# Kernel optimization log

Hardware: AMD Instinct MI355X
Metric: run time of the kernel (lower is better)

## Reference

```python
import jax, jax.numpy as jnp
import numpy as np

N_NODES = 50000
N_EDGES = 150000
N_GRAPHS = 1024
IN_DIM = 78
OUT_DIM = 64
HEADS = 10
HID = OUT_DIM * HEADS  # 640
NEG_SLOPE = 0.2


def _add_self_loops(edge_index, num_nodes):
    loop = jnp.arange(num_nodes, dtype=edge_index.dtype)
    src = jnp.concatenate([edge_index[0], loop])
    dst = jnp.concatenate([edge_index[1], loop])
    return src, dst


def gatv2_conv(x, edge_index, Wl, Wr, att, bias, heads, out_dim):
    # PyG GATv2Conv (share_weights=False, concat=True, add_self_loops=True),
    # inference mode so attention dropout is a no-op.
    N = x.shape[0]
    src, dst = _add_self_loops(edge_index, N)
    xl = (x @ Wl).reshape(N, heads, out_dim)  # source transform
    xr = (x @ Wr).reshape(N, heads, out_dim)  # target transform
    s = jax.nn.leaky_relu(xl[src] + xr[dst], NEG_SLOPE)      # [E,H,C]
    logits = jnp.einsum('ehc,hc->eh', s, att)                # [E,H]
    m = jax.ops.segment_max(logits, dst, num_segments=N)     # [N,H] (self-loops => no empty segs)
    ex = jnp.exp(logits - m[dst])
    den = jax.ops.segment_sum(ex, dst, num_segments=N)
    alpha = ex / den[dst]                                    # scatter-softmax over in-edges
    out = jax.ops.segment_sum(alpha[:, :, None] * xl[src], dst, num_segments=N)
    return out.reshape(N, heads * out_dim) + bias


def gcn_conv(x, edge_index, W, b):
    N = x.shape[0]
    src, dst = _add_self_loops(edge_index, N)
    deg = jax.ops.segment_sum(jnp.ones(src.shape[0], x.dtype), dst, num_segments=N)
    dinv = jax.lax.rsqrt(jnp.maximum(deg, 1.0))
    norm = dinv[src] * dinv[dst]                             # [E]
    xw = x @ W
    return jax.ops.segment_sum(norm[:, None] * xw[src], dst, num_segments=N) + b


def setup_inputs() -> dict:
    key = jax.random.key(0)
    ks = jax.random.split(key, 16)
    x = jax.random.normal(ks[0], (N_NODES, IN_DIM), dtype=jnp.float32)
    edge_index = jax.random.randint(ks[1], (2, N_EDGES), 0, N_NODES, dtype=jnp.int64)
    batch = jnp.sort(jax.random.randint(ks[2], (N_NODES,), 0, N_GRAPHS, dtype=jnp.int64))

    def glorot(k, shape, fan_in):
        return jax.random.normal(k, shape, dtype=jnp.float32) * (1.0 / np.sqrt(fan_in))

    return {
        'x': x, 'edge_index': edge_index, 'batch': batch,
        'Wl1': glorot(ks[3], (IN_DIM, HID), IN_DIM),
        'Wr1': glorot(ks[4], (IN_DIM, HID), IN_DIM),
        'a1': glorot(ks[5], (HEADS, OUT_DIM), OUT_DIM),
        'b1': jnp.zeros((HID,), jnp.float32),
        'Wl2': glorot(ks[6], (HID, HID), HID),
        'Wr2': glorot(ks[7], (HID, HID), HID),
        'a2': glorot(ks[8], (1, HID), HID),
        'b2': jnp.zeros((HID,), jnp.float32),
        'Wg': glorot(ks[9], (HID, HID), HID),
        'bg': jnp.zeros((HID,), jnp.float32),
    }


def reference(x, edge_index, batch, Wl1, Wr1, a1, b1, Wl2, Wr2, a2, b2, Wg, bg):
    # inference: feature dropout layers are identity
    h = jax.nn.elu(gatv2_conv(x, edge_index, Wl1, Wr1, a1, b1, HEADS, OUT_DIM))
    h = gatv2_conv(h, edge_index, Wl2, Wr2, a2, b2, 1, HID)
    h = gcn_conv(h, edge_index, Wg, bg)
    h = jax.nn.relu(h)
    # global max pool + global mean pool per graph
    gmax = jax.ops.segment_max(h, batch, num_segments=N_GRAPHS)
    cnt = jax.ops.segment_sum(jnp.ones((h.shape[0],), h.dtype), batch, num_segments=N_GRAPHS)
    gmean = jax.ops.segment_sum(h, batch, num_segments=N_GRAPHS) / jnp.maximum(cnt, 1.0)[:, None]
    return jnp.concatenate([gmax, gmean], axis=1)
```

## Files before the change

### kernel.cpp

```cpp
#include <hip/hip_runtime.h>
#include <hip/hip_bf16.h>
#include <cstdint>
#include <cstddef>

typedef __hip_bfloat16 bf16;

#define N_NODES  50000
#define N_EDGES  150000
#define E_TOT    (N_EDGES + N_NODES)
#define N_TILES  ((E_TOT + 15) / 16)
#define N_GRAPHS 1024
#define IN_DIM   78
#define K1P      128
#define OUT_DIM  64
#define HEADS    10
#define HID      640
#define NEG_SLOPE 0.2f
#define SCB      ((N_NODES + 255) / 256)

static __device__ __forceinline__ float b2f(bf16 v){ return __bfloat162float(v); }
static __device__ __forceinline__ bf16  f2b(float v){ return __float2bfloat16(v); }

__device__ __forceinline__ int clampi(int v, int hi){ return v < 0 ? 0 : (v >= hi ? hi - 1 : v); }

__device__ __forceinline__ float bf2f_bits(short s){
  return __uint_as_float(((unsigned)(unsigned short)s) << 16);
}
__device__ __forceinline__ short f2bf_bits(float v){
  unsigned u = __float_as_uint(v);
  return (short)((u + 0x7fffu + ((u >> 16) & 1u)) >> 16);
}
__device__ __forceinline__ short f2bf_trunc(float v){
  return (short)(__float_as_uint(v) >> 16);
}

__global__ __launch_bounds__(256) void fill_u32(unsigned* __restrict__ p, unsigned v, int n){
  int i = blockIdx.x * 256 + threadIdx.x;
  if (i < n) p[i] = v;
}

__global__ __launch_bounds__(256) void conv_x(const float* __restrict__ x, bf16* __restrict__ XB){
  int i = blockIdx.x * 256 + threadIdx.x;
  if (i >= N_NODES * K1P) return;
  int n = i / K1P, k = i - n * K1P;
  XB[i] = f2b(k < IN_DIM ? x[(size_t)n * IN_DIM + k] : 0.f);
}

__global__ __launch_bounds__(256) void conv_wT2(const float* __restrict__ W0,
                                                const float* __restrict__ W1,
                                                bf16* __restrict__ WT,
                                                int K, int N, int Kp){
  int i = blockIdx.x * 256 + threadIdx.x;
  const int per = N * Kp;
  if (i >= 2 * per) return;
  int m = i / per, r = i - m * per;
  const float* W = m == 0 ? W0 : W1;
  int n = r / Kp, k = r - n * Kp;
  WT[i] = f2b(k < K ? W[(size_t)k * N + n] : 0.f);
}

__global__ __launch_bounds__(256) void conv_wT3t(const float* __restrict__ W0,
                                                 const float* __restrict__ W1,
                                                 const float* __restrict__ W2,
                                                 bf16* __restrict__ WT){
  __shared__ float t[32][33];
  int m = blockIdx.z;
  const float* W = m == 0 ? W0 : (m == 1 ? W1 : W2);
  int n0 = blockIdx.x * 32, k0 = blockIdx.y * 32;
  int tx = threadIdx.x & 31, ty = threadIdx.x >> 5;
#pragma unroll
  for (int r = 0; r < 32; r += 8)
    t[ty + r][tx] = W[(size_t)(k0 + ty + r) * HID + n0 + tx];
  __syncthreads();
  bf16* O = WT + (size_t)m * HID * HID;
#pragma unroll
  for (int r = 0; r < 32; r += 8)
    O[(size_t)(n0 + ty + r) * HID + k0 + tx] = f2b(t[tx][ty + r]);
}

__global__ __launch_bounds__(256) void conv_attP(const float* __restrict__ a, bf16* __restrict__ P,
                                                 int heads){
  int i = blockIdx.x * 256 + threadIdx.x;
  if (i >= (HID / 32) * 512) return;
  int chunk = i >> 9;
  int lane  = (i >> 3) & 63;
  int j     = i & 7;
  int h = lane & 15;
  int k = (lane >> 4) * 8 + j;
  int c = chunk * 32 + k;
  float v = 0.f;
  if (heads == HEADS){ if (h < HEADS && (c >> 6) == h) v = a[c]; }
  else               { if (h == 0) v = a[c]; }
  P[i] = f2b(v);
}

#define BM 128
#define BN 128
#define BK 64

typedef __attribute__((ext_vector_type(8))) short bf16x8;
typedef __attribute__((ext_vector_type(4))) float f32x4;

typedef const __attribute__((address_space(1))) unsigned gu32;
typedef __attribute__((address_space(3))) unsigned lu32;

__global__ __launch_bounds__(256) void mfma_gemm(const bf16* __restrict__ A,
                                                 const bf16* __restrict__ BT,
                                                 bf16* __restrict__ C0,
                                                 bf16* __restrict__ C1,
                                                 int M, int Kp, int NB){
  int d   = blockIdx.x;
  int xcd = d & 7, j = d >> 3;
  int cb  = j % NB, ri = j / NB;
  int rb  = ri * 8 + xcd;
  const int row0 = rb * BM;
  if (row0 >= M) return;
  const int col0 = cb * BN;

  __shared__ short As[BM * BK];
  __shared__ short Bs[BN * BK];
  const int tid  = threadIdx.x;
  const int lane = tid & 63;
  const int wave = tid >> 6;
  const int wr   = (wave >> 1) * 64;
  const int wc   = (wave & 1) * 64;
  const int l15  = lane & 15;
  const int quad = lane >> 4;
  const int sw   = l15 & 7;

  const bf16* aptr[4];
  const bf16* bptr[4];
  lu32* lda[4];
  lu32* ldb[4];
#pragma unroll
  for (int t = 0; t < 4; ++t){
    int ci = (t * 4 + wave) * 64 + lane;
    int r  = ci >> 3;
    int sc = (ci & 7) ^ (r & 7);
    int gr = row0 + r; if (gr >= M) gr = M - 1;
    aptr[t] = A  + (size_t)gr * Kp + sc * 8;
    bptr[t] = BT + (size_t)(col0 + r) * Kp + sc * 8;
    lda[t]  = (lu32*)(&As[(t * 4 + wave) * 512]);
    ldb[t]  = (lu32*)(&Bs[(t * 4 + wave) * 512]);
  }

  f32x4 acc[4][4];
#pragma unroll
  for (int i = 0; i < 4; ++i)
#pragma unroll
    for (int jj = 0; jj < 4; ++jj) acc[i][jj] = (f32x4){0.f, 0.f, 0.f, 0.f};

  for (int k0 = 0; k0 < Kp; k0 += BK){
#pragma unroll
    for (int t = 0; t < 4; ++t){
      __builtin_amdgcn_global_load_lds((gu32*)(aptr[t] + k0), lda[t], 16, 0, 0);
      __builtin_amdgcn_global_load_lds((gu32*)(bptr[t] + k0), ldb[t], 16, 0, 0);
    }
    __syncthreads();

#pragma unroll
    for (int ks = 0; ks < 2; ++ks){
      const int slotA = ((ks * 4 + quad) ^ sw) * 8;
      bf16x8 af[4], bfr[4];
#pragma unroll
      for (int i = 0; i < 4; ++i)
        af[i] = *(bf16x8*)(&As[(wr + i * 16 + l15) * BK + slotA]);
#pragma unroll
      for (int jj = 0; jj < 4; ++jj)
        bfr[jj] = *(bf16x8*)(&Bs[(wc + jj * 16 + l15) * BK + slotA]);
#pragma unroll
      for (int i = 0; i < 4; ++i)
#pragma unroll
        for (int jj = 0; jj < 4; ++jj)
          acc[i][jj] = __builtin_amdgcn_mfma_f32_16x16x32_bf16(af[i], bfr[jj], acc[i][jj], 0, 0, 0);
    }
    __syncthreads();
  }

  if (row0 + BM <= M){
#pragma unroll
    for (int i = 0; i < 4; ++i){
#pragma unroll
      for (int jj = 0; jj < 4; ++jj){
        int gc = col0 + wc + jj * 16 + l15;
        bf16* Cp = (gc < HID) ? C0 : C1;
        size_t cc = (gc < HID) ? gc : gc - HID;
        size_t base = (size_t)(row0 + wr + i * 16 + quad * 4) * HID + cc;
#pragma unroll
        for (int r = 0; r < 4; ++r)
          Cp[base + (size_t)r * HID] = f2b(acc[i][jj][r]);
      }
    }
  } else {
#pragma unroll
    for (int i = 0; i < 4; ++i){
#pragma unroll
      for (int jj = 0; jj < 4; ++jj){
        int gc = col0 + wc + jj * 16 + l15;
        bf16* Cp = (gc < HID) ? C0 : C1;
        int cc   = (gc < HID) ? gc : gc - HID;
#pragma unroll
        for (int r = 0; r < 4; ++r){
          int gr = row0 + wr + i * 16 + quad * 4 + r;
          if (gr < M) Cp[(size_t)gr * HID + cc] = f2b(acc[i][jj][r]);
        }
      }
    }
  }
}

__global__ __launch_bounds__(256) void count_deg(const int* __restrict__ edst, int* __restrict__ degi){
  int e = blockIdx.x * 256 + threadIdx.x;
  if (e >= N_EDGES) return;
  atomicAdd(&degi[clampi(edst[e], N_NODES)], 1);
}

__global__ __launch_bounds__(256) void scan_blk(const int* __restrict__ degi,
                                                int* __restrict__ rowp,
                                                float* __restrict__ dinv,
                                                int* __restrict__ bsum){
  __shared__ int wsum[4];
  int b = blockIdx.x, tid = threadIdx.x;
  int i = b * 256 + tid;
  int lane = tid & 63, wv = tid >> 6;
  int v = (i < N_NODES) ? degi[i] : 0;
  int incl = v;
#pragma unroll
  for (int ofs = 1; ofs < 64; ofs <<= 1){
    int t = __shfl_up(incl, ofs);
    if (lane >= ofs) incl += t;
  }
  if (lane == 63) wsum[wv] = incl;
  __syncthreads();
  int woff = 0;
#pragma unroll
  for (int w = 0; w < 4; ++w) if (w < wv) woff += wsum[w];
  if (i < N_NODES){
    rowp[i] = woff + incl - v;
    dinv[i] = rsqrtf((float)(v + 1));
  }
  if (tid == 0) bsum[b] = wsum[0] + wsum[1] + wsum[2] + wsum[3];
}

__global__ __launch_bounds__(256) void scan_top(int* __restrict__ bsum, int* __restrict__ rowp){
  __shared__ int wsum[4];
  int tid = threadIdx.x, lane = tid & 63, wv = tid >> 6;
  int v = (tid < SCB) ? bsum[tid] : 0;
  int incl = v;
#pragma unroll
  for (int ofs = 1; ofs < 64; ofs <<= 1){
    int t = __shfl_up(incl, ofs);
    if (lane >= ofs) incl += t;
  }
  if (lane == 63) wsum[wv] = incl;
  __syncthreads();
  int woff = 0;
#pragma unroll
  for (int w = 0; w < 4; ++w) if (w < wv) woff += wsum[w];
  if (tid < SCB) bsum[tid] = woff + incl - v;
  if (tid == 255) rowp[N_NODES] = woff + incl;
}

__global__ __launch_bounds__(256) void scan_add(const int* __restrict__ bsum,
                                                int* __restrict__ rowp,
                                                int* __restrict__ curs){
  int i = blockIdx.x * 256 + threadIdx.x;
  if (i >= N_NODES) return;
  int r = rowp[i] + bsum[blockIdx.x];
  rowp[i] = r; curs[i] = r;
}

__global__ __launch_bounds__(256) void bucket_edges(const int* __restrict__ esrc,
                                                    const int* __restrict__ edst,
                                                    int* __restrict__ curs,
                                                    int* __restrict__ srcg,
                                                    int* __restrict__ dstg){
  int e = blockIdx.x * 256 + threadIdx.x;
  if (e >= N_EDGES) return;
  int d = clampi(edst[e], N_NODES);
  int pos = atomicAdd(&curs[d], 1);
  srcg[pos] = clampi(esrc[e], N_NODES);
  dstg[pos] = d;
}

__global__ __launch_bounds__(256) void logits_mfma(const bf16* __restrict__ xl,
                                                   const bf16* __restrict__ xr,
                                                   const int* __restrict__ srcg,
                                                   const int* __restrict__ dstg,
                                                   const bf16* __restrict__ attP,
                                                   float* __restrict__ LOG,
                                                   int only0){
  int wid  = (blockIdx.x * 256 + threadIdx.x) >> 6;
  int lane = threadIdx.x & 63;
  if (wid >= N_TILES) return;
  const int l15 = lane & 15, quad = lane >> 4;
  int p = wid * 16 + l15; if (p >= E_TOT) p = E_TOT - 1;
  int s, d;
  if (p < N_EDGES){ s = srcg[p]; d = dstg[p]; }
  else            { s = d = p - N_EDGES; }
  const bf16* ps = xl + (size_t)s * HID + quad * 8;
  const bf16* pd = xr + (size_t)d * HID + quad * 8;
  const bf16* pw = attP + lane * 8;

  f32x4 acc = (f32x4){0.f, 0.f, 0.f, 0.f};
  for (int k0 = 0; k0 < HID; k0 += 64){
    bf16x8 va0 = *(const bf16x8*)(ps + k0);
    bf16x8 vb0 = *(const bf16x8*)(pd + k0);
    bf16x8 va1 = *(const bf16x8*)(ps + k0 + 32);
    bf16x8 vb1 = *(const bf16x8*)(pd + k0 + 32);
    bf16x8 t0, t1;
#pragma unroll
    for (int j = 0; j < 8; ++j){
      float v0 = bf2f_bits(va0[j]) + bf2f_bits(vb0[j]);
      v0 *= (v0 > 0.f) ? 1.f : NEG_SLOPE;
      t0[j] = f2bf_trunc(v0);
      float v1 = bf2f_bits(va1[j]) + bf2f_bits(vb1[j]);
      v1 *= (v1 > 0.f) ? 1.f : NEG_SLOPE;
      t1[j] = f2bf_trunc(v1);
    }
    bf16x8 wb0 = *(const bf16x8*)(pw + (k0 >> 5) * 512);
    bf16x8 wb1 = *(const bf16x8*)(pw + ((k0 >> 5) + 1) * 512);
    acc = __builtin_amdgcn_mfma_f32_16x16x32_bf16(t0, wb0, acc, 0, 0, 0);
    acc = __builtin_amdgcn_mfma_f32_16x16x32_bf16(t1, wb1, acc, 0, 0, 0);
  }
  int er = wid * 16 + quad * 4;
  if (only0){
    if (l15 == 0){
#pragma unroll
      for (int r = 0; r < 4; ++r){
        int ee = er + r;
        if (ee < E_TOT) LOG[ee] = acc[r];
      }
    }
  } else {
#pragma unroll
    for (int r = 0; r < 4; ++r){
      int ee = er + r;
      if (ee < E_TOT) LOG[(size_t)ee * 16 + l15] = acc[r];
    }
  }
}

__global__ __launch_bounds__(256) void gat1_agg(const bf16* __restrict__ xl,
                                                const int* __restrict__ srcg,
                                                const int* __restrict__ rowp,
                                                const float* __restrict__ LOG,
                                                const float* __restrict__ bias,
                                                bf16* __restrict__ H){
  int n    = (blockIdx.x * 256 + threadIdx.x) >> 6;
  int lane = threadIdx.x & 63;
  if (n >= N_NODES) return;
  const int l15 = lane & 15;
  const int hA = lane >> 3;
  const int hB = 8 + (lane >> 5);
  int r0 = rowp[n], r1 = rowp[n + 1];

  float lself = LOG[(size_t)(N_EDGES + n) * 16 + l15];
  float m = lself;
  for (int p = r0; p < r1; ++p) m = fmaxf(m, LOG[(size_t)p * 16 + l15]);

  float p0  = __expf(lself - m);
  float den = p0;
  float accA[8], accB[2];
  {
    float pA = __shfl(p0, hA), pB = __shfl(p0, hB);
    const bf16* xn = xl + (size_t)n * HID;
    bf16x8 va = *(const bf16x8*)(xn + 8 * lane);
    unsigned vb = *(const unsigned*)(xn + 512 + 2 * lane);
#pragma unroll
    for (int j = 0; j < 8; ++j) accA[j] = pA * bf2f_bits(va[j]);
    accB[0] = pB * bf2f_bits((short)(vb & 0xffff));
    accB[1] = pB * bf2f_bits((short)(vb >> 16));
  }
  int p = r0;
  for (; p + 1 < r1; p += 2){
    int s0 = srcg[p], s1 = srcg[p + 1];
    float l0 = LOG[(size_t)p * 16 + l15];
    float l1 = LOG[(size_t)(p + 1) * 16 + l15];
    const bf16* xs0 = xl + (size_t)s0 * HID;
    const bf16* xs1 = xl + (size_t)s1 * HID;
    bf16x8 va0 = *(const bf16x8*)(xs0 + 8 * lane);
    bf16x8 va1 = *(const bf16x8*)(xs1 + 8 * lane);
    unsigned vb0 = *(const unsigned*)(xs0 + 512 + 2 * lane);
    unsigned vb1 = *(const unsigned*)(xs1 + 512 + 2 * lane);
    float pv0 = __expf(l0 - m), pv1 = __expf(l1 - m);
    den += pv0 + pv1;
    float pA0 = __shfl(pv0, hA), pB0 = __shfl(pv0, hB);
    float pA1 = __shfl(pv1, hA), pB1 = __shfl(pv1, hB);
#pragma unroll
    for (int j = 0; j < 8; ++j) accA[j] += pA0 * bf2f_bits(va0[j]) + pA1 * bf2f_bits(va1[j]);
    accB[0] += pB0 * bf2f_bits((short)(vb0 & 0xffff)) + pB1 * bf2f_bits((short)(vb1 & 0xffff));
    accB[1] += pB0 * bf2f_bits((short)(vb0 >> 16))    + pB1 * bf2f_bits((short)(vb1 >> 16));
  }
  if (p < r1){
    int s = srcg[p];
    float pv = __expf(LOG[(size_t)p * 16 + l15] - m);
    den += pv;
    float pA = __shfl(pv, hA), pB = __shfl(pv, hB);
    const bf16* xs = xl + (size_t)s * HID;
    bf16x8 va = *(const bf16x8*)(xs + 8 * lane);
    unsigned vb = *(const unsigned*)(xs + 512 + 2 * lane);
#pragma unroll
    for (int j = 0; j < 8; ++j) accA[j] += pA * bf2f_bits(va[j]);
    accB[0] += pB * bf2f_bits((short)(vb & 0xffff));
    accB[1] += pB * bf2f_bits((short)(vb >> 16));
  }
  float dA = __shfl(den, hA), dB = __shfl(den, hB);
  float4 bA0 = *(const float4*)(bias + 8 * lane);
  float4 bA1 = *(const float4*)(bias + 8 * lane + 4);
  float2 bB  = *(const float2*)(bias + 512 + 2 * lane);
  bf16x8 oA;
  float bAa[8] = {bA0.x, bA0.y, bA0.z, bA0.w, bA1.x, bA1.y, bA1.z, bA1.w};
#pragma unroll
  for (int j = 0; j < 8; ++j){
    float v = accA[j] / dA + bAa[j];
    v = v > 0.f ? v : (__expf(v) - 1.f);
    oA[j] = f2bf_bits(v);
  }
  float v0 = accB[0] / dB + bB.x; v0 = v0 > 0.f ? v0 : (__expf(v0) - 1.f);
  float v1 = accB[1] / dB + bB.y; v1 = v1 > 0.f ? v1 : (__expf(v1) - 1.f);
  bf16* hn = H + (size_t)n * HID;
  *(bf16x8*)(hn + 8 * lane) = oA;
  unsigned ob = (unsigned)(unsigned short)f2bf_bits(v0) |
                ((unsigned)(unsigned short)f2bf_bits(v1) << 16);
  *(unsigned*)(hn + 512 + 2 * lane) = ob;
}

__global__ __launch_bounds__(256) void gat2_agg(const bf16* __restrict__ xl,
                                                const int* __restrict__ srcg,
                                                const int* __restrict__ rowp,
                                                const float* __restrict__ LOG,
                                                const float* __restrict__ bias,
                                                bf16* __restrict__ H){
  int n    = (blockIdx.x * 256 + threadIdx.x) >> 6;
  int lane = threadIdx.x & 63;
  if (n >= N_NODES) return;
  int r0 = rowp[n], r1 = rowp[n + 1];

  float lself = LOG[N_EDGES + n];
  float m = lself;
  for (int p = r0; p < r1; ++p) m = fmaxf(m, LOG[p]);

  float p0  = __expf(lself - m);
  float den = p0;
  float accA[8], accB[2];
  {
    const bf16* xn = xl + (size_t)n * HID;
    bf16x8 va = *(const bf16x8*)(xn + 8 * lane);
    unsigned vb = *(const unsigned*)(xn + 512 + 2 * lane);
#pragma unroll
    for (int j = 0; j < 8; ++j) accA[j] = p0 * bf2f_bits(va[j]);
    accB[0] = p0 * bf2f_bits((short)(vb & 0xffff));
    accB[1] = p0 * bf2f_bits((short)(vb >> 16));
  }
  int p = r0;
  for (; p + 1 < r1; p += 2){
    int s0 = srcg[p], s1 = srcg[p + 1];
    float pv0 = __expf(LOG[p] - m), pv1 = __expf(LOG[p + 1] - m);
    const bf16* xs0 = xl + (size_t)s0 * HID;
    const bf16* xs1 = xl + (size_t)s1 * HID;
    bf16x8 va0 = *(const bf16x8*)(xs0 + 8 * lane);
    bf16x8 va1 = *(const bf16x8*)(xs1 + 8 * lane);
    unsigned vb0 = *(const unsigned*)(xs0 + 512 + 2 * lane);
    unsigned vb1 = *(const unsigned*)(xs1 + 512 + 2 * lane);
    den += pv0 + pv1;
#pragma unroll
    for (int j = 0; j < 8; ++j) accA[j] += pv0 * bf2f_bits(va0[j]) + pv1 * bf2f_bits(va1[j]);
    accB[0] += pv0 * bf2f_bits((short)(vb0 & 0xffff)) + pv1 * bf2f_bits((short)(vb1 & 0xffff));
    accB[1] += pv0 * bf2f_bits((short)(vb0 >> 16))    + pv1 * bf2f_bits((short)(vb1 >> 16));
  }
  if (p < r1){
    int s = srcg[p];
    float pv = __expf(LOG[p] - m);
    den += pv;
    const bf16* xs = xl + (size_t)s * HID;
    bf16x8 va = *(const bf16x8*)(xs + 8 * lane);
    unsigned vb = *(const unsigned*)(xs + 512 + 2 * lane);
#pragma unroll
    for (int j = 0; j < 8; ++j) accA[j] += pv * bf2f_bits(va[j]);
    accB[0] += pv * bf2f_bits((short)(vb & 0xffff));
    accB[1] += pv * bf2f_bits((short)(vb >> 16));
  }
  float inv = 1.f / den;
  float4 bA0 = *(const float4*)(bias + 8 * lane);
  float4 bA1 = *(const float4*)(bias + 8 * lane + 4);
  float2 bB  = *(const float2*)(bias + 512 + 2 * lane);
  float bAa[8] = {bA0.x, bA0.y, bA0.z, bA0.w, bA1.x, bA1.y, bA1.z, bA1.w};
  bf16x8 oA;
#pragma unroll
  for (int j = 0; j < 8; ++j) oA[j] = f2bf_bits(accA[j] * inv + bAa[j]);
  bf16* hn = H + (size_t)n * HID;
  *(bf16x8*)(hn + 8 * lane) = oA;
  unsigned ob = (unsigned)(unsigned short)f2bf_bits(accB[0] * inv + bB.x) |
                ((unsigned)(unsigned short)f2bf_bits(accB[1] * inv + bB.y) << 16);
  *(unsigned*)(hn + 512 + 2 * lane) = ob;
}

__global__ __launch_bounds__(256) void gcn_gather(const bf16* __restrict__ xw,
                                                  const int* __restrict__ srcg,
                                                  const int* __restrict__ rowp,
                                                  const float* __restrict__ dinv,
                                                  const float* __restrict__ bg,
                                                  bf16* __restrict__ h3){
  int n    = (blockIdx.x * 256 + threadIdx.x) >> 6;
  int lane = threadIdx.x & 63;
  if (n >= N_NODES) return;
  int r0 = rowp[n], r1 = rowp[n + 1];

  float dn = dinv[n];
  float accA[8], accB[2];
  {
    float w = dn * dn;
    const bf16* xn = xw + (size_t)n * HID;
    bf16x8 va = *(const bf16x8*)(xn + 8 * lane);
    unsigned vb = *(const unsigned*)(xn + 512 + 2 * lane);
#pragma unroll
    for (int j = 0; j < 8; ++j) accA[j] = w * bf2f_bits(va[j]);
    accB[0] = w * bf2f_bits((short)(vb & 0xffff));
    accB[1] = w * bf2f_bits((short)(vb >> 16));
  }
  int p = r0;
  for (; p + 1 < r1; p += 2){
    int s0 = srcg[p], s1 = srcg[p + 1];
    float w0 = dinv[s0] * dn, w1 = dinv[s1] * dn;
    const bf16* xs0 = xw + (size_t)s0 * HID;
    const bf16* xs1 = xw + (size_t)s1 * HID;
    bf16x8 va0 = *(const bf16x8*)(xs0 + 8 * lane);
    bf16x8 va1 = *(const bf16x8*)(xs1 + 8 * lane);
    unsigned vb0 = *(const unsigned*)(xs0 + 512 + 2 * lane);
    unsigned vb1 = *(const unsigned*)(xs1 + 512 + 2 * lane);
#pragma unroll
    for (int j = 0; j < 8; ++j) accA[j] += w0 * bf2f_bits(va0[j]) + w1 * bf2f_bits(va1[j]);
    accB[0] += w0 * bf2f_bits((short)(vb0 & 0xffff)) + w1 * bf2f_bits((short)(vb1 & 0xffff));
    accB[1] += w0 * bf2f_bits((short)(vb0 >> 16))    + w1 * bf2f_bits((short)(vb1 >> 16));
  }
  if (p < r1){
    int s = srcg[p];
    float w = dinv[s] * dn;
    const bf16* xs = xw + (size_t)s * HID;
    bf16x8 va = *(const bf16x8*)(xs + 8 * lane);
    unsigned vb = *(const unsigned*)(xs + 512 + 2 * lane);
#pragma unroll
    for (int j = 0; j < 8; ++j) accA[j] += w * bf2f_bits(va[j]);
    accB[0] += w * bf2f_bits((short)(vb & 0xffff));
    accB[1] += w * bf2f_bits((short)(vb >> 16));
  }
  float4 bA0 = *(const float4*)(bg + 8 * lane);
  float4 bA1 = *(const float4*)(bg + 8 * lane + 4);
  float2 bB  = *(const float2*)(bg + 512 + 2 * lane);
  float bAa[8] = {bA0.x, bA0.y, bA0.z, bA0.w, bA1.x, bA1.y, bA1.z, bA1.w};
  bf16x8 oA;
#pragma unroll
  for (int j = 0; j < 8; ++j) oA[j] = f2bf_bits(fmaxf(accA[j] + bAa[j], 0.f));
  bf16* hn = h3 + (size_t)n * HID;
  *(bf16x8*)(hn + 8 * lane) = oA;
  unsigned ob = (unsigned)(unsigned short)f2bf_bits(fmaxf(accB[0] + bB.x, 0.f)) |
                ((unsigned)(unsigned short)f2bf_bits(fmaxf(accB[1] + bB.y, 0.f)) << 16);
  *(unsigned*)(hn + 512 + 2 * lane) = ob;
}

__global__ __launch_bounds__(256) void graph_bounds(const int* __restrict__ batch,
                                                    int* __restrict__ gstart){
  int n = blockIdx.x * 256 + threadIdx.x;
  if (n >= N_NODES) return;
  int b = clampi(batch[n], N_GRAPHS);
  if (n == 0){
    for (int g = 0; g <= b; ++g) gstart[g] = 0;
  } else {
    int bp = clampi(batch[n - 1], N_GRAPHS);
    for (int g = bp + 1; g <= b; ++g) gstart[g] = n;
  }
  if (n == N_NODES - 1){
    for (int g = b + 1; g <= N_GRAPHS; ++g) gstart[g] = N_NODES;
  }
}

__global__ __launch_bounds__(640) void pool_graph(const bf16* __restrict__ h3,
                                                  const int* __restrict__ gstart,
                                                  float* __restrict__ out){
  int g = blockIdx.x;
  int c = threadIdx.x;
  int n0 = gstart[g], n1 = gstart[g + 1];
  float mx = 0.f, sm = 0.f;
  for (int n = n0; n < n1; ++n){
    float v = b2f(h3[(size_t)n * HID + c]);
    mx = fmaxf(mx, v); sm += v;
  }
  float mean = (n1 > n0) ? sm / (float)(n1 - n0) : 0.f;
  out[(size_t)g * 2 * HID + c]       = mx;
  out[(size_t)g * 2 * HID + HID + c] = mean;
}

extern "C" void kernel_launch(void* const* d_in, const int* in_sizes, int n_in,
                              void* d_out, int out_size, void* d_ws, size_t ws_size,
                              hipStream_t stream){
  const float* x     = (const float*)d_in[0];
  const int*   ei    = (const int*)d_in[1];
  const int*   batch = (const int*)d_in[2];
  const float* Wl1 = (const float*)d_in[3];
  const float* Wr1 = (const float*)d_in[4];
  const float* a1  = (const float*)d_in[5];
  const float* b1  = (const float*)d_in[6];
  const float* Wl2 = (const float*)d_in[7];
  const float* Wr2 = (const float*)d_in[8];
  const float* a2  = (const float*)d_in[9];
  const float* b2  = (const float*)d_in[10];
  const float* Wg  = (const float*)d_in[11];
  const float* bg  = (const float*)d_in[12];
  const int* esrc = ei;
  const int* edst = ei + N_EDGES;

  char* ws = (char*)d_ws;
  size_t off = 0;
  auto take = [&](size_t bytes)->char*{
    char* p = ws + off; off = (off + bytes + 255) & ~(size_t)255; return p;
  };
  bf16*     X1   = (bf16*)    take((size_t)N_NODES * HID * 2);
  bf16*     X2   = (bf16*)    take((size_t)N_NODES * HID * 2);
  bf16*     H    = (bf16*)    take((size_t)N_NODES * HID * 2);
  bf16*     XB   = (bf16*)    take((size_t)N_NODES * K1P * 2);
  bf16*     WT1l = (bf16*)    take((size_t)HID * K1P * 2);
  bf16*     WT1r = (bf16*)    take((size_t)HID * K1P * 2);
  bf16*     WT2l = (bf16*)    take((size_t)HID * HID * 2);
  bf16*     WT2r = (bf16*)    take((size_t)HID * HID * 2);
  bf16*     WTg  = (bf16*)    take((size_t)HID * HID * 2);
  bf16*     AT1P = (bf16*)    take((size_t)(HID / 32) * 512 * 2);
  bf16*     AT2P = (bf16*)    take((size_t)(HID / 32) * 512 * 2);
  float*    LOG  = (float*)   take((size_t)E_TOT * 16 * 4);
  int*      DEGI = (int*)     take((size_t)N_NODES * 4);
  int*      ROWP = (int*)     take((size_t)(N_NODES + 1) * 4);
  int*      CURS = (int*)     take((size_t)N_NODES * 4);
  int*      SRCG = (int*)     take((size_t)N_EDGES * 4);
  int*      DSTG = (int*)     take((size_t)N_EDGES * 4);
  float*    DINV = (float*)   take((size_t)N_NODES * 4);
  int*      GST  = (int*)     take((size_t)(N_GRAPHS + 1) * 4);
  int*      BSUM = (int*)     take((size_t)SCB * 4);

  dim3 blk(256);
  auto fill = [&](void* p, unsigned v, int n){
    fill_u32<<<dim3((n + 255) / 256), blk, 0, stream>>>((unsigned*)p, v, n);
  };
  const int MB8     = ((N_NODES + BM - 1) / BM + 7) / 8;
  const int nblocks = (N_NODES * 64 + 255) / 256;
  const int lblocks = (N_TILES * 64 + 255) / 256;
  const int reblk   = (N_EDGES + 255) / 256;
  const int apn     = (HID / 32) * 512;

  conv_x<<<(N_NODES * K1P + 255) / 256, blk, 0, stream>>>(x, XB);
  conv_wT2<<<(2 * HID * K1P + 255) / 256, blk, 0, stream>>>(Wl1, Wr1, WT1l, IN_DIM, HID, K1P);
  conv_wT3t<<<dim3(HID / 32, HID / 32, 3), blk, 0, stream>>>(Wl2, Wr2, Wg, WT2l);
  conv_attP<<<(apn + 255) / 256, blk, 0, stream>>>(a1, AT1P, HEADS);
  conv_attP<<<(apn + 255) / 256, blk, 0, stream>>>(a2, AT2P, 1);
  fill(DEGI, 0u, N_NODES);
  count_deg<<<reblk, blk, 0, stream>>>(edst, DEGI);
  scan_blk<<<dim3(SCB), blk, 0, stream>>>(DEGI, ROWP, DINV, BSUM);
  scan_top<<<dim3(1), blk, 0, stream>>>(BSUM, ROWP);
  scan_add<<<dim3(SCB), blk, 0, stream>>>(BSUM, ROWP, CURS);
  bucket_edges<<<reblk, blk, 0, stream>>>(esrc, edst, CURS, SRCG, DSTG);
  graph_bounds<<<(N_NODES + 255) / 256, blk, 0, stream>>>(batch, GST);

  mfma_gemm<<<dim3(8 * MB8 * 10), blk, 0, stream>>>(XB, WT1l, X1, X2, N_NODES, K1P, 10);
  logits_mfma<<<lblocks, blk, 0, stream>>>(X1, X2, SRCG, DSTG, AT1P, LOG, 0);
  gat1_agg<<<nblocks, blk, 0, stream>>>(X1, SRCG, ROWP, LOG, b1, H);

  mfma_gemm<<<dim3(8 * MB8 * 10), blk, 0, stream>>>(H, WT2l, X1, X2, N_NODES, HID, 10);
  logits_mfma<<<lblocks, blk, 0, stream>>>(X1, X2, SRCG, DSTG, AT2P, LOG, 1);
  gat2_agg<<<nblocks, blk, 0, stream>>>(X1, SRCG, ROWP, LOG, b2, H);

  mfma_gemm<<<dim3(8 * MB8 * 5), blk, 0, stream>>>(H, WTg, X1, X1, N_NODES, HID, 5);
  gcn_gather<<<nblocks, blk, 0, stream>>>(X1, SRCG, ROWP, DINV, bg, X2);
  pool_graph<<<dim3(N_GRAPHS), dim3(640), 0, stream>>>(X2, GST, (float*)d_out);
}
```

Measured before the change: 608.4 us.

## Fuse GCN neighbour gather with per-graph max/mean pooling

Replaces the separate GCN gather kernel and pool kernel with one kernel that runs one block per graph, computes each node's normalized neighbour sum per channel and immediately folds it into the running max and mean. This avoids writing and re-reading the intermediate node-feature matrix and saves a launch. In exchange, parallelism drops to 1024 blocks that walk their nodes serially, loads become 2-byte per-thread scalar reads instead of vectorized ones, and per-edge index loads are repeated across all channel threads, so latency exposure grows.

```diff
diff --git a/kernel.cpp b/kernel.cpp
--- a/kernel.cpp
+++ b/kernel.cpp
@@ -496,67 +496,34 @@
   *(unsigned*)(hn + 512 + 2 * lane) = ob;
 }
 
-__global__ __launch_bounds__(256) void gcn_gather(const bf16* __restrict__ xw,
-                                                  const int* __restrict__ srcg,
-                                                  const int* __restrict__ rowp,
-                                                  const float* __restrict__ dinv,
-                                                  const float* __restrict__ bg,
-                                                  bf16* __restrict__ h3){
-  int n    = (blockIdx.x * 256 + threadIdx.x) >> 6;
-  int lane = threadIdx.x & 63;
-  if (n >= N_NODES) return;
-  int r0 = rowp[n], r1 = rowp[n + 1];
-
-  float dn = dinv[n];
-  float accA[8], accB[2];
-  {
-    float w = dn * dn;
-    const bf16* xn = xw + (size_t)n * HID;
-    bf16x8 va = *(const bf16x8*)(xn + 8 * lane);
-    unsigned vb = *(const unsigned*)(xn + 512 + 2 * lane);
-#pragma unroll
-    for (int j = 0; j < 8; ++j) accA[j] = w * bf2f_bits(va[j]);
-    accB[0] = w * bf2f_bits((short)(vb & 0xffff));
-    accB[1] = w * bf2f_bits((short)(vb >> 16));
-  }
-  int p = r0;
-  for (; p + 1 < r1; p += 2){
-    int s0 = srcg[p], s1 = srcg[p + 1];
-    float w0 = dinv[s0] * dn, w1 = dinv[s1] * dn;
-    const bf16* xs0 = xw + (size_t)s0 * HID;
-    const bf16* xs1 = xw + (size_t)s1 * HID;
-    bf16x8 va0 = *(const bf16x8*)(xs0 + 8 * lane);
-    bf16x8 va1 = *(const bf16x8*)(xs1 + 8 * lane);
-    unsigned vb0 = *(const unsigned*)(xs0 + 512 + 2 * lane);
-    unsigned vb1 = *(const unsigned*)(xs1 + 512 + 2 * lane);
-#pragma unroll
-    for (int j = 0; j < 8; ++j) accA[j] += w0 * bf2f_bits(va0[j]) + w1 * bf2f_bits(va1[j]);
-    accB[0] += w0 * bf2f_bits((short)(vb0 & 0xffff)) + w1 * bf2f_bits((short)(vb1 & 0xffff));
-    accB[1] += w0 * bf2f_bits((short)(vb0 >> 16))    + w1 * bf2f_bits((short)(vb1 >> 16));
-  }
-  if (p < r1){
-    int s = srcg[p];
-    float w = dinv[s] * dn;
-    const bf16* xs = xw + (size_t)s * HID;
-    bf16x8 va = *(const bf16x8*)(xs + 8 * lane);
-    unsigned vb = *(const unsigned*)(xs + 512 + 2 * lane);
-#pragma unroll
-    for (int j = 0; j < 8; ++j) accA[j] += w * bf2f_bits(va[j]);
-    accB[0] += w * bf2f_bits((short)(vb & 0xffff));
-    accB[1] += w * bf2f_bits((short)(vb >> 16));
-  }
-  float4 bA0 = *(const float4*)(bg + 8 * lane);
-  float4 bA1 = *(const float4*)(bg + 8 * lane + 4);
-  float2 bB  = *(const float2*)(bg + 512 + 2 * lane);
-  float bAa[8] = {bA0.x, bA0.y, bA0.z, bA0.w, bA1.x, bA1.y, bA1.z, bA1.w};
-  bf16x8 oA;
-#pragma unroll
-  for (int j = 0; j < 8; ++j) oA[j] = f2bf_bits(fmaxf(accA[j] + bAa[j], 0.f));
-  bf16* hn = h3 + (size_t)n * HID;
-  *(bf16x8*)(hn + 8 * lane) = oA;
-  unsigned ob = (unsigned)(unsigned short)f2bf_bits(fmaxf(accB[0] + bB.x, 0.f)) |
-                ((unsigned)(unsigned short)f2bf_bits(fmaxf(accB[1] + bB.y, 0.f)) << 16);
-  *(unsigned*)(hn + 512 + 2 * lane) = ob;
+__global__ __launch_bounds__(640) void gcn_pool(const bf16* __restrict__ xw,
+                                                const int* __restrict__ srcg,
+                                                const int* __restrict__ rowp,
+                                                const float* __restrict__ dinv,
+                                                const float* __restrict__ bg,
+                                                const int* __restrict__ gstart,
+                                                float* __restrict__ out){
+  int g = blockIdx.x;
+  int c = threadIdx.x;
+  int n0 = gstart[g], n1 = gstart[g + 1];
+  float bc = bg[c];
+  float mx = 0.f, sm = 0.f;
+  const short* xs = (const short*)xw;
+  for (int n = n0; n < n1; ++n){
+    int r0 = rowp[n], r1 = rowp[n + 1];
+    float dn = dinv[n];
+    float acc = dn * dn * bf2f_bits(xs[(size_t)n * HID + c]);
+    for (int p = r0; p < r1; ++p){
+      int s = srcg[p];
+      acc += dinv[s] * dn * bf2f_bits(xs[(size_t)s * HID + c]);
+    }
+    float v = fmaxf(acc + bc, 0.f);
+    mx = fmaxf(mx, v);
+    sm += v;
+  }
+  float mean = (n1 > n0) ? sm / (float)(n1 - n0) : 0.f;
+  out[(size_t)g * 2 * HID + c]       = mx;
+  out[(size_t)g * 2 * HID + HID + c] = mean;
 }
 
 __global__ __launch_bounds__(256) void graph_bounds(const int* __restrict__ batch,
@@ -573,22 +540,6 @@
   if (n == N_NODES - 1){
     for (int g = b + 1; g <= N_GRAPHS; ++g) gstart[g] = N_NODES;
   }
-}
-
-__global__ __launch_bounds__(640) void pool_graph(const bf16* __restrict__ h3,
-                                                  const int* __restrict__ gstart,
-                                                  float* __restrict__ out){
-  int g = blockIdx.x;
-  int c = threadIdx.x;
-  int n0 = gstart[g], n1 = gstart[g + 1];
-  float mx = 0.f, sm = 0.f;
-  for (int n = n0; n < n1; ++n){
-    float v = b2f(h3[(size_t)n * HID + c]);
-    mx = fmaxf(mx, v); sm += v;
-  }
-  float mean = (n1 > n0) ? sm / (float)(n1 - n0) : 0.f;
-  out[(size_t)g * 2 * HID + c]       = mx;
-  out[(size_t)g * 2 * HID + HID + c] = mean;
 }
 
 extern "C" void kernel_launch(void* const* d_in, const int* in_sizes, int n_in,
@@ -668,6 +619,5 @@
   gat2_agg<<<nblocks, blk, 0, stream>>>(X1, SRCG, ROWP, LOG, b2, H);
 
   mfma_gemm<<<dim3(8 * MB8 * 5), blk, 0, stream>>>(H, WTg, X1, X1, N_NODES, HID, 5);
-  gcn_gather<<<nblocks, blk, 0, stream>>>(X1, SRCG, ROWP, DINV, bg, X2);
-  pool_graph<<<dim3(N_GRAPHS), dim3(640), 0, stream>>>(X2, GST, (float*)d_out);
-}
+  gcn_pool<<<dim3(N_GRAPHS), dim3(640), 0, stream>>>(X1, SRCG, ROWP, DINV, bg, GST, (float*)d_out);
+}
```

New measurement: 677.6 us. 11.4% more time.
